# Kernel optimization log

Hardware: AMD Instinct MI355X
Metric: run time of the kernel (lower is better)

## Reference

```python
import jax, jax.numpy as jnp
import numpy as np

N, E, K, F_IN, H = 50000, 640000, 3, 128, 128


def setup_inputs() -> dict:
    key = jax.random.key(0)
    ks = jax.random.split(key, 14)
    s = 0.05
    return {
        "x": jax.random.normal(ks[0], (N, F_IN), jnp.float32),
        "edge_index": jax.random.randint(ks[1], (2, E), 0, N, dtype=jnp.int32),
        "edge_weight": jax.random.uniform(ks[2], (E,), jnp.float32, minval=0.1, maxval=1.0),
        "W_x": jax.random.normal(ks[3], (4, F_IN, H), jnp.float32) * s,   # dense input weights (i,f,c,o)
        "w_c": jax.random.normal(ks[4], (3, H), jnp.float32) * s,         # peephole weights (i,f,o)
        "b": jax.random.normal(ks[5], (4, H), jnp.float32) * s,           # gate biases (i,f,c,o)
        "theta": jax.random.normal(ks[6], (4, K, H, H), jnp.float32) * s, # ChebConv weights per gate
        "theta_b": jax.random.normal(ks[7], (4, H), jnp.float32) * s,     # ChebConv biases per gate
        "gcn_w": jax.random.normal(ks[8], (H, H), jnp.float32) * s,
        "gcn_b": jnp.zeros((H,), jnp.float32),
        "bn_gamma": jnp.ones((H,), jnp.float32),
        "bn_beta": jnp.zeros((H,), jnp.float32),
        "bn_mean": jax.random.normal(ks[9], (H,), jnp.float32) * 0.1,
        "bn_var": jax.random.uniform(ks[10], (H,), jnp.float32, minval=0.5, maxval=1.5),
        "lin_w": jax.random.normal(ks[11], (H, 1), jnp.float32) * s,
        "lin_b": jnp.zeros((1,), jnp.float32),
    }


def reference(x, edge_index, edge_weight, W_x, w_c, b, theta, theta_b, gcn_w, gcn_b, bn_gamma, bn_beta, bn_mean, bn_var, lin_w, lin_b):
    n = x.shape[0]
    src, dst = edge_index[0], edge_index[1]

    # --- ChebConv normalization (sym, lambda_max=2): L_hat = -D^{-1/2} A D^{-1/2}, zero diagonal ---
    deg = jnp.zeros((n,), x.dtype).at[src].add(edge_weight)
    safe = jnp.where(deg > 0, deg, 1.0)
    dis = jnp.where(deg > 0, jax.lax.rsqrt(safe), 0.0)
    lw = -dis[src] * edge_weight * dis[dst]  # per-edge scaled-Laplacian weight

    def prop(h):  # out[i] = sum_{edges j->i} lw * h[j]
        return jnp.zeros_like(h).at[dst].add(lw[:, None] * h[src])

    def cheb(h, th, tb):  # sum_k T_k(L_hat) h @ theta_k + bias, Chebyshev recurrence
        Tx0, out = h, h @ th[0]
        Tx1 = prop(h)
        out = out + Tx1 @ th[1]
        for k in range(2, K):
            Tx2 = 2.0 * prop(Tx1) - Tx0
            out = out + Tx2 @ th[k]
            Tx0, Tx1 = Tx1, Tx2
        return out + tb

    # --- GCLSTM with H = C = 0 (module passes no initial state) ---
    Hs = jnp.zeros((n, W_x.shape[2]), x.dtype)
    Cs = jnp.zeros_like(Hs)
    I = jax.nn.sigmoid(x @ W_x[0] + cheb(Hs, theta[0], theta_b[0]) + w_c[0] * Cs + b[0])
    Fg = jax.nn.sigmoid(x @ W_x[1] + cheb(Hs, theta[1], theta_b[1]) + w_c[1] * Cs + b[1])
    T = jnp.tanh(x @ W_x[2] + cheb(Hs, theta[2], theta_b[2]) + b[2])
    Cs = Fg * Cs + I * T
    O = jax.nn.sigmoid(x @ W_x[3] + cheb(Hs, theta[3], theta_b[3]) + w_c[2] * Cs + b[3])
    Hs = O * jnp.tanh(Cs)

    # --- GCNConv(H) with unit edge weights + added self-loops ---
    h = Hs @ gcn_w
    deg_g = jnp.ones((n,), x.dtype).at[dst].add(jnp.ones((edge_index.shape[1],), x.dtype))
    dg = jax.lax.rsqrt(deg_g)
    g = jnp.zeros_like(h).at[dst].add((dg[src] * dg[dst])[:, None] * h[src]) + (dg * dg)[:, None] * h + gcn_b

    g = jax.nn.relu(g)
    g = bn_gamma * (g - bn_mean) * jax.lax.rsqrt(bn_var + 1e-5) + bn_beta  # BatchNorm1d (eval)
    return g @ lin_w + lin_b  # Dropout = identity in eval
```

## Files before the change

### kernel.cpp

```cpp
#include <hip/hip_runtime.h>
#include <hip/hip_bf16.h>

#define NN 50000
#define NE 640000
#define NP 196
#define CAP 64
#define NGB 782
#define NFB 625

typedef unsigned short ushort_t;
typedef unsigned int uint_t;
typedef __attribute__((ext_vector_type(8))) short bf16x8;
typedef __attribute__((ext_vector_type(4))) float f32x4;

__device__ __forceinline__ float b2f(ushort_t u) {
    union { uint_t u; float f; } v; v.u = ((uint_t)u) << 16; return v.f;
}
__device__ __forceinline__ ushort_t f2b(float f) {
    union { float f; uint_t u; } v; v.f = f;
    uint_t u = v.u;
    uint_t r = u + 0x7fffu + ((u >> 16) & 1u);
    return (ushort_t)(r >> 16);
}
__device__ __forceinline__ float fsig(float x)  { return __builtin_amdgcn_rcpf(1.0f + __expf(-x)); }
__device__ __forceinline__ float ftanh(float x) { return 1.0f - 2.0f * __builtin_amdgcn_rcpf(1.0f + __expf(2.0f * x)); }
__device__ __forceinline__ float ldm(const void* p, int i, int mf) {
    return mf ? ((const float*)p)[i] : b2f(((const ushort_t*)p)[i]);
}

#define OFF_HB   0
#define OFF_BSRC 12800000
#define OFF_CNT  25600000
#define OFF_WT   25800000
#define OFF_COEF 25931072
#define OFF_MODE 25933640
#define WS_REQ   25933648

__global__ void fb_k(ushort_t* __restrict__ out, int n) {
    int i = blockIdx.x * blockDim.x + threadIdx.x;
    if (i < n) out[i] = 0;
}

__global__ void init_k(const ushort_t* __restrict__ x, int* __restrict__ cnt,
                       int* __restrict__ mode) {
    __shared__ int s[256];
    int b = blockIdx.x, t = threadIdx.x;
    if (b < NP) {
        int i = b * 256 + t;
        if (i < NN) cnt[i] = 0;
    } else {
        int bad = 0;
        for (int i = t; i < 4096; i += 256) {
            int e = (x[i] >> 7) & 0xFF;
            if (e >= 0xC0) bad++;
        }
        s[t] = bad; __syncthreads();
        for (int o = 128; o >= 1; o >>= 1) { if (t < o) s[t] += s[t + o]; __syncthreads(); }
        if (t == 0) mode[0] = (s[0] > 8) ? 1 : 0;
    }
}

__global__ void prep_k(const void* __restrict__ Wx, const void* __restrict__ gcnw,
                       const void* __restrict__ wc, const void* __restrict__ bb,
                       const void* __restrict__ thb,
                       const void* __restrict__ gam, const void* __restrict__ bet,
                       const void* __restrict__ mea, const void* __restrict__ var,
                       const void* __restrict__ linw, const void* __restrict__ linb,
                       const int* __restrict__ mode,
                       ushort_t* __restrict__ WT, float* __restrict__ coef) {
    __shared__ float red[128];
    int b = blockIdx.x, t = threadIdx.x;
    int mf = mode[0];
    if (b < 32) {
        int gid = b * 256 + t;
        int m  = gid >> 11;
        int u  = gid & 2047;
        int k  = u >> 4;
        int f0 = (u & 15) << 3;
        const int srcoff[4] = { 0, 2 * 16384, 3 * 16384, 0 };
        const void* S = (m == 3) ? gcnw : Wx;
        int sbase = srcoff[m] + k * 128 + f0;
        ushort_t vals[8];
        if (mf == 0) {
            bf16x8 v = *(const bf16x8*)((const ushort_t*)S + sbase);
            #pragma unroll
            for (int i = 0; i < 8; i++) vals[i] = (ushort_t)v[i];
        } else {
            const float* Sf = (const float*)S + sbase;
            #pragma unroll
            for (int i = 0; i < 8; i++) vals[i] = f2b(Sf[i]);
        }
        ushort_t* D = WT + m * 16384 + k;
        #pragma unroll
        for (int i = 0; i < 8; i++) D[(f0 + i) * 128] = vals[i];
    } else {
        if (t < 128) {
            float rs = rsqrtf(ldm(var, t, mf) + 1e-5f);
            float ga = ldm(gam, t, mf);
            float lw = ldm(linw, t, mf);
            coef[t]       = ldm(thb, t, mf)           + ldm(bb, t, mf);
            coef[128 + t] = ldm(thb, 2 * 128 + t, mf) + ldm(bb, 2 * 128 + t, mf);
            coef[256 + t] = ldm(thb, 3 * 128 + t, mf) + ldm(bb, 3 * 128 + t, mf);
            coef[384 + t] = ldm(wc, 2 * 128 + t, mf);
            coef[512 + t] = ga * rs * lw;
            red[t] = (ldm(bet, t, mf) - ldm(mea, t, mf) * ga * rs) * lw;
        }
        __syncthreads();
        for (int off = 64; off >= 1; off >>= 1) {
            if (t < off && t < 128) red[t] += red[t + off];
            __syncthreads();
        }
        if (t == 0) coef[640] = red[0] + ldm(linb, 0, mf);
    }
}

__launch_bounds__(256)
__global__ void gafi_k(const void* __restrict__ x, const ushort_t* __restrict__ WT,
                       const float* __restrict__ coef, const int* __restrict__ mode,
                       ushort_t* __restrict__ hb,
                       const int* __restrict__ ei, int* __restrict__ cnt,
                       int* __restrict__ bsrc) {
    __shared__ ushort_t tile[64 * 136];
    int per = blockIdx.x / 9, rem = blockIdx.x % 9;
    int t = threadIdx.x;

    if (rem >= 5) {
        int fb = per * 4 + (rem - 5);
        if (fb >= NFB) return;
        int tid = fb * 256 + t;
        int4 s4 = ((const int4*)ei)[tid];
        int4 d4 = ((const int4*)(ei + NE))[tid];
        int p0 = atomicAdd(&cnt[d4.x], 1);
        int p1 = atomicAdd(&cnt[d4.y], 1);
        int p2 = atomicAdd(&cnt[d4.z], 1);
        int p3 = atomicAdd(&cnt[d4.w], 1);
        if (p0 < CAP) bsrc[d4.x * CAP + p0] = s4.x;
        if (p1 < CAP) bsrc[d4.y * CAP + p1] = s4.y;
        if (p2 < CAP) bsrc[d4.z * CAP + p2] = s4.z;
        if (p3 < CAP) bsrc[d4.w * CAP + p3] = s4.w;
        return;
    }

    int gb = per * 5 + rem;
    if (gb >= NGB) return;
    int base = gb * 64;
    int mf = mode[0];

    for (int i = 0; i < 4; i++) {
        int idx = (i * 256 + t) * 8;
        int row = idx >> 7, col = idx & 127;
        int n = base + row;
        bf16x8 v;
        if (n >= NN) {
            v = (bf16x8)0;
        } else if (mf == 0) {
            v = *(const bf16x8*)((const ushort_t*)x + n * 128 + col);
        } else {
            const float* xf = (const float*)x + n * 128 + col;
            float4 lo = *(const float4*)xf;
            float4 hi = *(const float4*)(xf + 4);
            v[0] = (short)f2b(lo.x); v[1] = (short)f2b(lo.y);
            v[2] = (short)f2b(lo.z); v[3] = (short)f2b(lo.w);
            v[4] = (short)f2b(hi.x); v[5] = (short)f2b(hi.y);
            v[6] = (short)f2b(hi.z); v[7] = (short)f2b(hi.w);
        }
        *(bf16x8*)&tile[row * 136 + col] = v;
    }
    __syncthreads();

    int lane = t & 63, wave = t >> 6;
    int m = lane & 15, quad = lane >> 4;

    bf16x8 a[4][4];
    #pragma unroll
    for (int rt = 0; rt < 4; rt++)
        #pragma unroll
        for (int kt = 0; kt < 4; kt++)
            a[rt][kt] = *(const bf16x8*)&tile[(rt * 16 + m) * 136 + kt * 32 + quad * 8];
    __syncthreads();

    const ushort_t* WTi = WT;
    const ushort_t* WTc = WT + 16384;
    const ushort_t* WTo = WT + 2 * 16384;

    #pragma unroll
    for (int ft = 0; ft < 2; ft++) {
        int f = wave * 32 + ft * 16 + m;
        bf16x8 bi[4], bc[4], bo[4];
        #pragma unroll
        for (int kt = 0; kt < 4; kt++) {
            int off = f * 128 + kt * 32 + quad * 8;
            bi[kt] = *(const bf16x8*)(WTi + off);
            bc[kt] = *(const bf16x8*)(WTc + off);
            bo[kt] = *(const bf16x8*)(WTo + off);
        }
        float bi_f = coef[f], bc_f = coef[128 + f], bo_f = coef[256 + f], w2 = coef[384 + f];
        #pragma unroll
        for (int rt = 0; rt < 4; rt++) {
            f32x4 ai = {0,0,0,0}, ac = {0,0,0,0}, ao = {0,0,0,0};
            #pragma unroll
            for (int kt = 0; kt < 4; kt++) {
                ai = __builtin_amdgcn_mfma_f32_16x16x32_bf16(a[rt][kt], bi[kt], ai, 0, 0, 0);
                ac = __builtin_amdgcn_mfma_f32_16x16x32_bf16(a[rt][kt], bc[kt], ac, 0, 0, 0);
                ao = __builtin_amdgcn_mfma_f32_16x16x32_bf16(a[rt][kt], bo[kt], ao, 0, 0, 0);
            }
            #pragma unroll
            for (int r = 0; r < 4; r++) {
                float I  = fsig(ai[r] + bi_f);
                float T  = ftanh(ac[r] + bc_f);
                float Cs = I * T;
                float O  = fsig(ao[r] + w2 * Cs + bo_f);
                float Hs = O * ftanh(Cs);
                tile[(rt * 16 + quad * 4 + r) * 136 + f] = f2b(Hs);
            }
        }
    }
    __syncthreads();

    const ushort_t* WTg = WT + 3 * 16384;
    bf16x8 ah[4][4];
    #pragma unroll
    for (int rt = 0; rt < 4; rt++)
        #pragma unroll
        for (int kt = 0; kt < 4; kt++)
            ah[rt][kt] = *(const bf16x8*)&tile[(rt * 16 + m) * 136 + kt * 32 + quad * 8];

    #pragma unroll
    for (int ft = 0; ft < 2; ft++) {
        int f = wave * 32 + ft * 16 + m;
        bf16x8 bg[4];
        #pragma unroll
        for (int kt = 0; kt < 4; kt++)
            bg[kt] = *(const bf16x8*)(WTg + f * 128 + kt * 32 + quad * 8);
        #pragma unroll
        for (int rt = 0; rt < 4; rt++) {
            f32x4 acc = {0,0,0,0};
            #pragma unroll
            for (int kt = 0; kt < 4; kt++)
                acc = __builtin_amdgcn_mfma_f32_16x16x32_bf16(ah[rt][kt], bg[kt], acc, 0, 0, 0);
            #pragma unroll
            for (int r = 0; r < 4; r++) {
                int n = base + rt * 16 + quad * 4 + r;
                if (n < NN) hb[n * 128 + f] = f2b(acc[r]);
            }
        }
    }
}

__launch_bounds__(256)
__global__ void gat_out_k(const ushort_t* __restrict__ hb, const int* __restrict__ cnt,
                          const int* __restrict__ bsrc,
                          const void* __restrict__ gcnb, const float* __restrict__ coef,
                          const int* __restrict__ mode, void* __restrict__ out) {
    int wid  = (blockIdx.x * blockDim.x + threadIdx.x) >> 6;
    int lane = threadIdx.x & 63;
    if (wid >= NN) return;
    int half = lane >> 5, sl = lane & 31;
    int c = cnt[wid]; if (c < 0) c = 0;
    int deg = (c < CAP) ? c : CAP;
    const int* brow = bsrc + wid * CAP;

    float a0 = 0.0f, a1 = 0.0f, a2 = 0.0f, a3 = 0.0f;
    int s0 = brow[half];
    int s1 = brow[half + 2];
    for (int j = half; j < deg; j += 4) {
        int sn0 = brow[(j + 4) & (CAP - 1)];
        int sn1 = brow[(j + 6) & (CAP - 1)];
        {
            int cs = cnt[s0]; if (cs < 0) cs = 0;
            uint2 r = *(const uint2*)(hb + s0 * 128 + sl * 4);
            float w = rsqrtf(1.0f + (float)cs);
            a0 += w * b2f((ushort_t)(r.x & 0xffffu));
            a1 += w * b2f((ushort_t)(r.x >> 16));
            a2 += w * b2f((ushort_t)(r.y & 0xffffu));
            a3 += w * b2f((ushort_t)(r.y >> 16));
        }
        if (j + 2 < deg) {
            int cs = cnt[s1]; if (cs < 0) cs = 0;
            uint2 r = *(const uint2*)(hb + s1 * 128 + sl * 4);
            float w = rsqrtf(1.0f + (float)cs);
            a0 += w * b2f((ushort_t)(r.x & 0xffffu));
            a1 += w * b2f((ushort_t)(r.x >> 16));
            a2 += w * b2f((ushort_t)(r.y & 0xffffu));
            a3 += w * b2f((ushort_t)(r.y >> 16));
        }
        s0 = sn0; s1 = sn1;
    }
    float d = rsqrtf(1.0f + (float)c);
    if (half == 0) {
        uint2 r = *(const uint2*)(hb + wid * 128 + sl * 4);
        a0 += d * b2f((ushort_t)(r.x & 0xffffu));
        a1 += d * b2f((ushort_t)(r.x >> 16));
        a2 += d * b2f((ushort_t)(r.y & 0xffffu));
        a3 += d * b2f((ushort_t)(r.y >> 16));
    }
    a0 += __shfl_xor(a0, 32); a1 += __shfl_xor(a1, 32);
    a2 += __shfl_xor(a2, 32); a3 += __shfl_xor(a3, 32);
    int mf = mode[0];
    int fb = sl * 4;
    float g0 = d * a0 + ldm(gcnb, fb,     mf);
    float g1 = d * a1 + ldm(gcnb, fb + 1, mf);
    float g2 = d * a2 + ldm(gcnb, fb + 2, mf);
    float g3 = d * a3 + ldm(gcnb, fb + 3, mf);
    float v = fmaxf(g0, 0.0f) * coef[512 + fb]
            + fmaxf(g1, 0.0f) * coef[512 + fb + 1]
            + fmaxf(g2, 0.0f) * coef[512 + fb + 2]
            + fmaxf(g3, 0.0f) * coef[512 + fb + 3];
    #pragma unroll
    for (int o = 32; o >= 1; o >>= 1) v += __shfl_down(v, o);
    if (lane == 0) {
        float r = 0.5f * v + coef[640];
        if (mf) ((float*)out)[wid] = r;
        else    ((ushort_t*)out)[wid] = f2b(r);
    }
}

extern "C" void kernel_launch(void* const* d_in, const int* in_sizes, int n_in,
                              void* d_out, int out_size, void* d_ws, size_t ws_size,
                              hipStream_t stream) {
    if (ws_size < (size_t)WS_REQ) {
        fb_k<<<(out_size + 255) / 256, 256, 0, stream>>>((ushort_t*)d_out, out_size);
        return;
    }
    const void* x    = d_in[0];
    const int*  ei   = (const int*)d_in[1];
    const void* Wx   = d_in[3];
    const void* wc   = d_in[4];
    const void* bb   = d_in[5];
    const void* thb  = d_in[7];
    const void* gcnw = d_in[8];
    const void* gcnb = d_in[9];
    const void* gam  = d_in[10];
    const void* bet  = d_in[11];
    const void* mea  = d_in[12];
    const void* var  = d_in[13];
    const void* linw = d_in[14];
    const void* linb = d_in[15];

    char* ws = (char*)d_ws;
    ushort_t* hb   = (ushort_t*)(ws + OFF_HB);
    int*      bsrc = (int*)     (ws + OFF_BSRC);
    int*      cnt  = (int*)     (ws + OFF_CNT);
    ushort_t* WT   = (ushort_t*)(ws + OFF_WT);
    float*    coef = (float*)   (ws + OFF_COEF);
    int*      mode = (int*)     (ws + OFF_MODE);

    init_k<<<NP + 1, 256, 0, stream>>>((const ushort_t*)x, cnt, mode);
    prep_k<<<33, 256, 0, stream>>>(Wx, gcnw, wc, bb, thb, gam, bet, mea, var, linw, linb, mode, WT, coef);
    gafi_k<<<157 * 9, 256, 0, stream>>>(x, WT, coef, mode, hb, ei, cnt, bsrc);
    gat_out_k<<<(NN * 64 + 255) / 256, 256, 0, stream>>>(hb, cnt, bsrc, gcnb, coef, mode, d_out);
}
```

Before: 190.3 us.

## Interleave edge bucket fill into GEMM blocks and unroll gather loop by four

The fused kernel no longer uses separate blocks for the edge bucketing. Each of the first 625 GEMM blocks now loads its edge chunk early, issues the count atomics before the gate MFMAs, and writes the bucket entries after them, so atomic latency is hidden behind matrix work and the grid shrinks to 782 blocks. The gather kernel's loop is also rewritten to process four independent edges per half-wave per iteration without software prefetch, which exposes more memory-level parallelism. The costs are fewer total blocks for the fill work, higher register pressure from holding the edge data across the GEMM, and predicated loads wasted on the last iteration of the gather loop.

```diff
diff --git a/kernel.cpp b/kernel.cpp
--- a/kernel.cpp
+++ b/kernel.cpp
@@ -6,7 +6,6 @@
 #define NP 196
 #define CAP 64
 #define NGB 782
-#define NFB 625
 
 typedef unsigned short ushort_t;
 typedef unsigned int uint_t;
@@ -121,31 +120,17 @@
                        const int* __restrict__ ei, int* __restrict__ cnt,
                        int* __restrict__ bsrc) {
     __shared__ ushort_t tile[64 * 136];
-    int per = blockIdx.x / 9, rem = blockIdx.x % 9;
-    int t = threadIdx.x;
-
-    if (rem >= 5) {
-        int fb = per * 4 + (rem - 5);
-        if (fb >= NFB) return;
-        int tid = fb * 256 + t;
-        int4 s4 = ((const int4*)ei)[tid];
-        int4 d4 = ((const int4*)(ei + NE))[tid];
-        int p0 = atomicAdd(&cnt[d4.x], 1);
-        int p1 = atomicAdd(&cnt[d4.y], 1);
-        int p2 = atomicAdd(&cnt[d4.z], 1);
-        int p3 = atomicAdd(&cnt[d4.w], 1);
-        if (p0 < CAP) bsrc[d4.x * CAP + p0] = s4.x;
-        if (p1 < CAP) bsrc[d4.y * CAP + p1] = s4.y;
-        if (p2 < CAP) bsrc[d4.z * CAP + p2] = s4.z;
-        if (p3 < CAP) bsrc[d4.w * CAP + p3] = s4.w;
-        return;
-    }
-
-    int gb = per * 5 + rem;
-    if (gb >= NGB) return;
-    int base = gb * 64;
+    int b = blockIdx.x, t = threadIdx.x;
+    bool doFill = (b < 625);
+    int4 s4, d4;
+    if (doFill) {
+        int tid = b * 256 + t;
+        s4 = ((const int4*)ei)[tid];
+        d4 = ((const int4*)(ei + NE))[tid];
+    }
+
+    int base = b * 64;
     int mf = mode[0];
-
     for (int i = 0; i < 4; i++) {
         int idx = (i * 256 + t) * 8;
         int row = idx >> 7, col = idx & 127;
@@ -179,6 +164,14 @@
             a[rt][kt] = *(const bf16x8*)&tile[(rt * 16 + m) * 136 + kt * 32 + quad * 8];
     __syncthreads();
 
+    int p0, p1, p2, p3;
+    if (doFill) {
+        p0 = atomicAdd(&cnt[d4.x], 1);
+        p1 = atomicAdd(&cnt[d4.y], 1);
+        p2 = atomicAdd(&cnt[d4.z], 1);
+        p3 = atomicAdd(&cnt[d4.w], 1);
+    }
+
     const ushort_t* WTi = WT;
     const ushort_t* WTc = WT + 16384;
     const ushort_t* WTo = WT + 2 * 16384;
@@ -216,6 +209,13 @@
         }
     }
     __syncthreads();
+
+    if (doFill) {
+        if (p0 < CAP) bsrc[d4.x * CAP + p0] = s4.x;
+        if (p1 < CAP) bsrc[d4.y * CAP + p1] = s4.y;
+        if (p2 < CAP) bsrc[d4.z * CAP + p2] = s4.z;
+        if (p3 < CAP) bsrc[d4.w * CAP + p3] = s4.w;
+    }
 
     const ushort_t* WTg = WT + 3 * 16384;
     bf16x8 ah[4][4];
@@ -261,31 +261,24 @@
     const int* brow = bsrc + wid * CAP;
 
     float a0 = 0.0f, a1 = 0.0f, a2 = 0.0f, a3 = 0.0f;
-    int s0 = brow[half];
-    int s1 = brow[half + 2];
-    for (int j = half; j < deg; j += 4) {
-        int sn0 = brow[(j + 4) & (CAP - 1)];
-        int sn1 = brow[(j + 6) & (CAP - 1)];
-        {
-            int cs = cnt[s0]; if (cs < 0) cs = 0;
-            uint2 r = *(const uint2*)(hb + s0 * 128 + sl * 4);
-            float w = rsqrtf(1.0f + (float)cs);
-            a0 += w * b2f((ushort_t)(r.x & 0xffffu));
-            a1 += w * b2f((ushort_t)(r.x >> 16));
-            a2 += w * b2f((ushort_t)(r.y & 0xffffu));
-            a3 += w * b2f((ushort_t)(r.y >> 16));
-        }
-        if (j + 2 < deg) {
-            int cs = cnt[s1]; if (cs < 0) cs = 0;
-            uint2 r = *(const uint2*)(hb + s1 * 128 + sl * 4);
-            float w = rsqrtf(1.0f + (float)cs);
-            a0 += w * b2f((ushort_t)(r.x & 0xffffu));
-            a1 += w * b2f((ushort_t)(r.x >> 16));
-            a2 += w * b2f((ushort_t)(r.y & 0xffffu));
-            a3 += w * b2f((ushort_t)(r.y >> 16));
-        }
-        s0 = sn0; s1 = sn1;
-    }
+    #define EDGE(idx_expr)  do { int _j = (idx_expr); \
+        int _s = brow[_j & (CAP - 1)]; \
+        if (_j < deg) { \
+            int _cs = cnt[_s]; if (_cs < 0) _cs = 0; \
+            uint2 _r = *(const uint2*)(hb + _s * 128 + sl * 4); \
+            float _w = rsqrtf(1.0f + (float)_cs); \
+            a0 += _w * b2f((ushort_t)(_r.x & 0xffffu)); \
+            a1 += _w * b2f((ushort_t)(_r.x >> 16)); \
+            a2 += _w * b2f((ushort_t)(_r.y & 0xffffu)); \
+            a3 += _w * b2f((ushort_t)(_r.y >> 16)); } } while (0)
+
+    for (int jj = 0; jj < deg; jj += 8) {
+        EDGE(jj + half);
+        EDGE(jj + half + 2);
+        EDGE(jj + half + 4);
+        EDGE(jj + half + 6);
+    }
+    #undef EDGE
     float d = rsqrtf(1.0f + (float)c);
     if (half == 0) {
         uint2 r = *(const uint2*)(hb + wid * 128 + sl * 4);
@@ -347,6 +340,6 @@
 
     init_k<<<NP + 1, 256, 0, stream>>>((const ushort_t*)x, cnt, mode);
     prep_k<<<33, 256, 0, stream>>>(Wx, gcnw, wc, bb, thb, gam, bet, mea, var, linw, linb, mode, WT, coef);
-    gafi_k<<<157 * 9, 256, 0, stream>>>(x, WT, coef, mode, hb, ei, cnt, bsrc);
+    gafi_k<<<NGB, 256, 0, stream>>>(x, WT, coef, mode, hb, ei, cnt, bsrc);
     gat_out_k<<<(NN * 64 + 255) / 256, 256, 0, stream>>>(hb, cnt, bsrc, gcnb, coef, mode, d_out);
 }
```

After: 204.1 us. +7.3%, slower.

## Interleave edge bucket fill into GEMM blocks and pad per-node counters

Applied to the files above, without the earlier changes.

Instead of dedicating separate blocks to the edge scatter, every one of the first 625 GEMM blocks now loads its edge indices up front, issues the count atomics after the tile load, and writes the bucket entries after the gate compute. The atomic latency is meant to hide behind the MFMA work. Each counter is also placed on its own 64-byte slot (stride 16 ints) to cut atomic contention between neighbouring nodes. In exchange the counter array grows 16x, and the count reads in the gather kernel become strided, which hurts cache locality.

```diff
diff --git a/kernel.cpp b/kernel.cpp
--- a/kernel.cpp
+++ b/kernel.cpp
@@ -6,7 +6,7 @@
 #define NP 196
 #define CAP 64
 #define NGB 782
-#define NFB 625
+#define CS  16
 
 typedef unsigned short ushort_t;
 typedef unsigned int uint_t;
@@ -31,10 +31,10 @@
 #define OFF_HB   0
 #define OFF_BSRC 12800000
 #define OFF_CNT  25600000
-#define OFF_WT   25800000
-#define OFF_COEF 25931072
-#define OFF_MODE 25933640
-#define WS_REQ   25933648
+#define OFF_WT   28800000
+#define OFF_COEF 28931072
+#define OFF_MODE 28933640
+#define WS_REQ   28933648
 
 __global__ void fb_k(ushort_t* __restrict__ out, int n) {
     int i = blockIdx.x * blockDim.x + threadIdx.x;
@@ -47,7 +47,7 @@
     int b = blockIdx.x, t = threadIdx.x;
     if (b < NP) {
         int i = b * 256 + t;
-        if (i < NN) cnt[i] = 0;
+        if (i < NN) cnt[i * CS] = 0;
     } else {
         int bad = 0;
         for (int i = t; i < 4096; i += 256) {
@@ -121,31 +121,17 @@
                        const int* __restrict__ ei, int* __restrict__ cnt,
                        int* __restrict__ bsrc) {
     __shared__ ushort_t tile[64 * 136];
-    int per = blockIdx.x / 9, rem = blockIdx.x % 9;
-    int t = threadIdx.x;
-
-    if (rem >= 5) {
-        int fb = per * 4 + (rem - 5);
-        if (fb >= NFB) return;
-        int tid = fb * 256 + t;
-        int4 s4 = ((const int4*)ei)[tid];
-        int4 d4 = ((const int4*)(ei + NE))[tid];
-        int p0 = atomicAdd(&cnt[d4.x], 1);
-        int p1 = atomicAdd(&cnt[d4.y], 1);
-        int p2 = atomicAdd(&cnt[d4.z], 1);
-        int p3 = atomicAdd(&cnt[d4.w], 1);
-        if (p0 < CAP) bsrc[d4.x * CAP + p0] = s4.x;
-        if (p1 < CAP) bsrc[d4.y * CAP + p1] = s4.y;
-        if (p2 < CAP) bsrc[d4.z * CAP + p2] = s4.z;
-        if (p3 < CAP) bsrc[d4.w * CAP + p3] = s4.w;
-        return;
-    }
-
-    int gb = per * 5 + rem;
-    if (gb >= NGB) return;
-    int base = gb * 64;
+    int b = blockIdx.x, t = threadIdx.x;
+    bool doFill = (b < 625);
+    int4 s4, d4;
+    if (doFill) {
+        int tid = b * 256 + t;
+        s4 = ((const int4*)ei)[tid];
+        d4 = ((const int4*)(ei + NE))[tid];
+    }
+
+    int base = b * 64;
     int mf = mode[0];
-
     for (int i = 0; i < 4; i++) {
         int idx = (i * 256 + t) * 8;
         int row = idx >> 7, col = idx & 127;
@@ -179,6 +165,14 @@
             a[rt][kt] = *(const bf16x8*)&tile[(rt * 16 + m) * 136 + kt * 32 + quad * 8];
     __syncthreads();
 
+    int p0, p1, p2, p3;
+    if (doFill) {
+        p0 = atomicAdd(&cnt[d4.x * CS], 1);
+        p1 = atomicAdd(&cnt[d4.y * CS], 1);
+        p2 = atomicAdd(&cnt[d4.z * CS], 1);
+        p3 = atomicAdd(&cnt[d4.w * CS], 1);
+    }
+
     const ushort_t* WTi = WT;
     const ushort_t* WTc = WT + 16384;
     const ushort_t* WTo = WT + 2 * 16384;
@@ -216,6 +210,13 @@
         }
     }
     __syncthreads();
+
+    if (doFill) {
+        if (p0 < CAP) bsrc[d4.x * CAP + p0] = s4.x;
+        if (p1 < CAP) bsrc[d4.y * CAP + p1] = s4.y;
+        if (p2 < CAP) bsrc[d4.z * CAP + p2] = s4.z;
+        if (p3 < CAP) bsrc[d4.w * CAP + p3] = s4.w;
+    }
 
     const ushort_t* WTg = WT + 3 * 16384;
     bf16x8 ah[4][4];
@@ -256,7 +257,7 @@
     int lane = threadIdx.x & 63;
     if (wid >= NN) return;
     int half = lane >> 5, sl = lane & 31;
-    int c = cnt[wid]; if (c < 0) c = 0;
+    int c = cnt[wid * CS]; if (c < 0) c = 0;
     int deg = (c < CAP) ? c : CAP;
     const int* brow = bsrc + wid * CAP;
 
@@ -267,7 +268,7 @@
         int sn0 = brow[(j + 4) & (CAP - 1)];
         int sn1 = brow[(j + 6) & (CAP - 1)];
         {
-            int cs = cnt[s0]; if (cs < 0) cs = 0;
+            int cs = cnt[s0 * CS]; if (cs < 0) cs = 0;
             uint2 r = *(const uint2*)(hb + s0 * 128 + sl * 4);
             float w = rsqrtf(1.0f + (float)cs);
             a0 += w * b2f((ushort_t)(r.x & 0xffffu));
@@ -276,7 +277,7 @@
             a3 += w * b2f((ushort_t)(r.y >> 16));
         }
         if (j + 2 < deg) {
-            int cs = cnt[s1]; if (cs < 0) cs = 0;
+            int cs = cnt[s1 * CS]; if (cs < 0) cs = 0;
             uint2 r = *(const uint2*)(hb + s1 * 128 + sl * 4);
             float w = rsqrtf(1.0f + (float)cs);
             a0 += w * b2f((ushort_t)(r.x & 0xffffu));
@@ -347,6 +348,6 @@
 
     init_k<<<NP + 1, 256, 0, stream>>>((const ushort_t*)x, cnt, mode);
     prep_k<<<33, 256, 0, stream>>>(Wx, gcnw, wc, bb, thb, gam, bet, mea, var, linw, linb, mode, WT, coef);
-    gafi_k<<<157 * 9, 256, 0, stream>>>(x, WT, coef, mode, hb, ei, cnt, bsrc);
+    gafi_k<<<NGB, 256, 0, stream>>>(x, WT, coef, mode, hb, ei, cnt, bsrc);
     gat_out_k<<<(NN * 64 + 255) / 256, 256, 0, stream>>>(hb, cnt, bsrc, gcnb, coef, mode, d_out);
 }
```

New measurement: 190.9 us. About the same (+0.3%).
